# Optimization experiments

Hardware: AMD Instinct MI355X
Metric: run time of the kernel (lower is better)

Reference implementation:

```python
import jax, jax.numpy as jnp
import numpy as np
import math

B, S, D = 4, 4096, 2048
HEAD_DIM = 128  # dim_model // head_nums = 2048 // 16
DEPTH = 12


def setup_inputs() -> dict:
    key = jax.random.key(0)
    ks = jax.random.split(key, 8)
    std = 0.1
    return {
        "x": jax.random.normal(ks[0], (B, S, D), dtype=jnp.float32),
        "WQ": jax.random.normal(ks[1], (D, 2 * HEAD_DIM), dtype=jnp.float32) * (D ** -0.5),
        "WK": jax.random.normal(ks[2], (D, 2 * HEAD_DIM), dtype=jnp.float32) * (D ** -0.5),
        "WV": jax.random.normal(ks[3], (D, 2 * HEAD_DIM), dtype=jnp.float32) * (D ** -0.5),
        "lambda_q1": jax.random.normal(ks[4], (HEAD_DIM,), dtype=jnp.float32) * std,
        "lambda_q2": jax.random.normal(ks[5], (HEAD_DIM,), dtype=jnp.float32) * std,
        "lambda_k1": jax.random.normal(ks[6], (HEAD_DIM,), dtype=jnp.float32) * std,
        "lambda_k2": jax.random.normal(ks[7], (HEAD_DIM,), dtype=jnp.float32) * std,
    }


def reference(x, WQ, WK, WV, lambda_q1, lambda_q2, lambda_k1, lambda_k2):
    scale = HEAD_DIM ** -0.5
    lambda_init = 0.8 - 0.6 * math.exp(-0.3 * DEPTH)

    q = x @ WQ                      # [B, S, 2*hd]
    k = x @ WK
    v = x @ WV                      # [B, S, 2*hd]
    q1, q2 = q[..., :HEAD_DIM], q[..., HEAD_DIM:]
    k1, k2 = k[..., :HEAD_DIM], k[..., HEAD_DIM:]

    a1 = jnp.einsum("bqd,bkd->bqk", q1, k1) * scale  # [B, S, S]
    a2 = jnp.einsum("bqd,bkd->bqk", q2, k2) * scale

    lambda_1 = jnp.exp(jnp.sum(lambda_q1 * lambda_k1))
    lambda_2 = jnp.exp(jnp.sum(lambda_q2 * lambda_k2))
    lam = lambda_1 + lambda_2 + lambda_init

    attn = jax.nn.softmax(a1, axis=-1) - lam * jax.nn.softmax(a2, axis=-1)
    return jnp.einsum("bqk,bkd->bqd", attn, v)  # [B, S, 2*hd]
```

## Files before the change

kernel.cpp:

```cpp
#include <hip/hip_runtime.h>
#include <stdint.h>

typedef unsigned short u16;
typedef __attribute__((ext_vector_type(4))) float f32x4;
typedef __attribute__((ext_vector_type(16))) float f32x16;
typedef __attribute__((ext_vector_type(8))) short s16x8;
typedef __attribute__((ext_vector_type(8))) __bf16 bf16x8;
typedef __attribute__((ext_vector_type(8))) unsigned short u16x8;
typedef __attribute__((ext_vector_type(4))) unsigned short u16x4;

__device__ __forceinline__ f32x4 mfma16(s16x8 a, s16x8 b, f32x4 c) {
  return __builtin_amdgcn_mfma_f32_16x16x32_bf16(
      __builtin_bit_cast(bf16x8, a), __builtin_bit_cast(bf16x8, b), c, 0, 0, 0);
}
__device__ __forceinline__ f32x16 mfma32(s16x8 a, s16x8 b, f32x16 c) {
  return __builtin_amdgcn_mfma_f32_32x32x16_bf16(
      __builtin_bit_cast(bf16x8, a), __builtin_bit_cast(bf16x8, b), c, 0, 0, 0);
}

__device__ __forceinline__ void gl_lds16(const u16* g, u16* l) {
  __builtin_amdgcn_global_load_lds(
      (const __attribute__((address_space(1))) void*)g,
      (__attribute__((address_space(3))) void*)l, 16, 0, 0);
}

__device__ __forceinline__ u16 bf16rne(float f) {
  uint32_t u = __builtin_bit_cast(uint32_t, f);
  u += 0x7fffu + ((u >> 16) & 1u);
  return (u16)(u >> 16);
}

__global__ void cast_x_kernel(const float* __restrict__ x, u16* __restrict__ xb) {
  size_t i = ((size_t)blockIdx.x * 256 + threadIdx.x) * 8;
  f32x4 a = *(const f32x4*)(x + i);
  f32x4 b = *(const f32x4*)(x + i + 4);
  u16x8 o;
#pragma unroll
  for (int j = 0; j < 4; ++j) { o[j] = bf16rne(a[j]); o[4 + j] = bf16rne(b[j]); }
  *(u16x8*)(xb + i) = o;
}

__global__ void cast_w_kernel(const float* __restrict__ WQ, const float* __restrict__ WK,
                              const float* __restrict__ WV, u16* __restrict__ Wt, float qscale) {
  int i = blockIdx.x * 256 + threadIdx.x;
  int r = i >> 11, k = i & 2047;
  int sel = r >> 8, c = r & 255;
  const float* W = (sel == 0) ? WQ : (sel == 1) ? WK : WV;
  float v = W[(size_t)k * 256 + c];
  if (sel == 0) v *= qscale;
  Wt[i] = bf16rne(v);
}

__global__ __launch_bounds__(256) void proj_gemm(const u16* __restrict__ xb, const u16* __restrict__ Wt,
                                                 u16* __restrict__ Qb, u16* __restrict__ Kb,
                                                 u16* __restrict__ Vt) {
  const int bid = blockIdx.x;
  const int xcd = bid & 7, j = bid >> 3;
  const int m0 = (xcd * 16 + (j / 6)) * 128;
  const int n0 = (j % 6) * 128;
  const int tid = threadIdx.x, lane = tid & 63, w = tid >> 6;
  const int ln = lane & 15, quad = lane >> 4;
  const int wm = w & 1, wn = w >> 1;
  __shared__ __align__(16) u16 As[128 * 32];
  __shared__ __align__(16) u16 Bs[128 * 32];
  f32x4 acc[4][4];
#pragma unroll
  for (int i = 0; i < 4; ++i)
#pragma unroll
    for (int jj = 0; jj < 4; ++jj) acc[i][jj] = f32x4{0.f, 0.f, 0.f, 0.f};

  for (int kk = 0; kk < 2048; kk += 32) {
    __syncthreads();
#pragma unroll
    for (int i = 0; i < 2; ++i) {
      int p = tid + i * 256;
      int row = p >> 2, cg = (p & 3) ^ (row & 3);
      gl_lds16(xb + (size_t)(m0 + row) * 2048 + kk + cg * 8, As + (size_t)(p - lane) * 8);
      gl_lds16(Wt + (size_t)(n0 + row) * 2048 + kk + cg * 8, Bs + (size_t)(p - lane) * 8);
    }
    __syncthreads();
    s16x8 a[4];
#pragma unroll
    for (int mt = 0; mt < 4; ++mt) {
      int r = wm * 64 + mt * 16 + ln;
      a[mt] = *(const s16x8*)(As + r * 32 + ((quad ^ (r & 3)) * 8));
    }
#pragma unroll
    for (int nt = 0; nt < 4; ++nt) {
      int r = wn * 64 + nt * 16 + ln;
      s16x8 bf = *(const s16x8*)(Bs + r * 32 + ((quad ^ (r & 3)) * 8));
#pragma unroll
      for (int mt = 0; mt < 4; ++mt) acc[mt][nt] = mfma16(a[mt], bf, acc[mt][nt]);
    }
  }
#pragma unroll
  for (int mt = 0; mt < 4; ++mt)
#pragma unroll
    for (int nt = 0; nt < 4; ++nt) {
      int row0 = m0 + wm * 64 + mt * 16 + quad * 4;
      int col = n0 + wn * 64 + nt * 16 + ln;
      int sel = col >> 8, c = col & 255;
      u16x4 vv;
#pragma unroll
      for (int jj = 0; jj < 4; ++jj) vv[jj] = bf16rne(acc[mt][nt][jj]);
      if (sel == 2) {
        int b = row0 >> 12, s = row0 & 4095;
        *(u16x4*)(Vt + (size_t)b * 1048576 + (size_t)c * 4096 + s) = vv;
      } else {
        u16* dst = (sel == 0) ? Qb : Kb;
#pragma unroll
        for (int jj = 0; jj < 4; ++jj) dst[(size_t)(row0 + jj) * 256 + c] = vv[jj];
      }
    }
}

__global__ void lam_kernel(const float* __restrict__ lq1, const float* __restrict__ lq2,
                           const float* __restrict__ lk1, const float* __restrict__ lk2,
                           float* __restrict__ lamp) {
  int t = threadIdx.x;
  float d1 = lq1[t] * lk1[t] + lq1[t + 64] * lk1[t + 64];
  float d2 = lq2[t] * lk2[t] + lq2[t + 64] * lk2[t + 64];
#pragma unroll
  for (int off = 32; off; off >>= 1) {
    d1 += __shfl_xor(d1, off);
    d2 += __shfl_xor(d2, off);
  }
  if (t == 0) *lamp = expf(d1) + expf(d2) + (0.8f - 0.6f * expf(-3.6f));
}

__global__ __launch_bounds__(256, 2) void attn_kernel(const u16* __restrict__ Qb,
                                                      const u16* __restrict__ Kb,
                                                      const u16* __restrict__ Vt,
                                                      float* __restrict__ Op,
                                                      float* __restrict__ lp) {
  const int qt = blockIdx.x, half = blockIdx.y, b = blockIdx.z;
  const int tid = threadIdx.x, lane = tid & 63, w = tid >> 6;
  const int l5 = lane & 31, lh = lane >> 5;
  const int mapsel = w & 1, rt = w >> 1;

  __shared__ __align__(16) u16 Ks[64 * 256];
  __shared__ __align__(16) u16 Vs[256 * 64];
  u16* Ps = Ks;

  s16x8 aq[8];
  {
    const u16* qp = Qb + ((size_t)(b * 4096 + qt * 64 + rt * 32 + l5)) * 256 +
                    mapsel * 128 + lh * 8;
#pragma unroll
    for (int st = 0; st < 8; ++st) aq[st] = *(const s16x8*)(qp + st * 16);
  }

  f32x16 O[2][4];
#pragma unroll
  for (int i = 0; i < 2; ++i)
#pragma unroll
    for (int jj = 0; jj < 4; ++jj)
#pragma unroll
      for (int r = 0; r < 16; ++r) O[i][jj][r] = 0.f;
  float l_run[16];
#pragma unroll
  for (int r = 0; r < 16; ++r) l_run[r] = 0.f;

  const u16* Kg0 = Kb + ((size_t)b * 4096) * 256;
  const u16* Vg0 = Vt + (size_t)b * 1048576;
  const int kb0 = half * 2048;

  for (int kb = kb0; kb < kb0 + 2048; kb += 64) {
    __syncthreads();
#pragma unroll
    for (int i = 0; i < 8; ++i) {
      int p = tid + i * 256;
      int row = p >> 5, c = p & 31;
      int cg = (c & 16) | ((c ^ row) & 15);
      gl_lds16(Kg0 + (size_t)(kb + row) * 256 + cg * 8, Ks + (size_t)(p - lane) * 8);
    }
#pragma unroll
    for (int i = 0; i < 8; ++i) {
      int p = tid + i * 256;
      int row = p >> 3, c = p & 7;
      int cg = c ^ (row & 7);
      gl_lds16(Vg0 + (size_t)row * 4096 + kb + cg * 8, Vs + (size_t)(p - lane) * 8);
    }
    __syncthreads();

    f32x16 S0, S1;
#pragma unroll
    for (int r = 0; r < 16; ++r) { S0[r] = 0.f; S1[r] = 0.f; }
#pragma unroll
    for (int st = 0; st < 8; ++st) {
      int c = mapsel * 16 + st * 2 + lh;
      int ph0 = (c & 16) | ((c ^ l5) & 15);
      s16x8 b0 = *(const s16x8*)(Ks + l5 * 256 + ph0 * 8);
      s16x8 b1 = *(const s16x8*)(Ks + (32 + l5) * 256 + ph0 * 8);
      S0 = mfma32(aq[st], b0, S0);
      S1 = mfma32(aq[st], b1, S1);
    }

    __syncthreads();
    {
      int qbase = mapsel * 64 + rt * 32 + 4 * lh;
#pragma unroll
      for (int r = 0; r < 16; ++r) {
        float p0 = exp2f(S0[r]);
        float p1 = exp2f(S1[r]);
        l_run[r] += p0 + p1;
        int qrow = qbase + (r & 3) + 8 * (r >> 2);
        Ps[qrow * 72 + l5] = bf16rne(p0);
        Ps[qrow * 72 + 32 + l5] = bf16rne(p1);
      }
    }
    __syncthreads();

#pragma unroll
    for (int ks = 0; ks < 4; ++ks) {
      s16x8 ap0 = *(const s16x8*)(Ps + (mapsel * 64 + l5) * 72 + ks * 16 + lh * 8);
      s16x8 ap1 = *(const s16x8*)(Ps + (mapsel * 64 + 32 + l5) * 72 + ks * 16 + lh * 8);
      int c = ks * 2 + lh;
#pragma unroll
      for (int ct = 0; ct < 4; ++ct) {
        int n = (w >> 1) * 128 + ct * 32 + l5;
        s16x8 bv = *(const s16x8*)(Vs + n * 64 + ((c ^ (n & 7)) * 8));
        O[0][ct] = mfma32(ap0, bv, O[0][ct]);
        O[1][ct] = mfma32(ap1, bv, O[1][ct]);
      }
    }
  }

#pragma unroll
  for (int off = 16; off; off >>= 1)
#pragma unroll
    for (int r = 0; r < 16; ++r) l_run[r] += __shfl_xor(l_run[r], off);

  const int mh = mapsel * 2 + half;
  const size_t MS = (size_t)16384 * 256;
  float* Og = Op + (size_t)mh * MS + (size_t)b * 4096 * 256;
  float* lg = lp + (size_t)mh * 16384 + (size_t)b * 4096;
  if (l5 == 0) {
#pragma unroll
    for (int r = 0; r < 16; ++r) {
      int qg = qt * 64 + rt * 32 + 4 * lh + (r & 3) + 8 * (r >> 2);
      lg[qg] = l_run[r];
    }
  }
#pragma unroll
  for (int rt2 = 0; rt2 < 2; ++rt2)
#pragma unroll
    for (int ct = 0; ct < 4; ++ct)
#pragma unroll
      for (int r = 0; r < 16; ++r) {
        int qg = qt * 64 + rt2 * 32 + (r & 3) + 8 * (r >> 2) + 4 * lh;
        int col = (w >> 1) * 128 + ct * 32 + l5;
        Og[(size_t)qg * 256 + col] = O[rt2][ct][r];
      }
}

__global__ void combine_kernel(const float* __restrict__ Op, const float* __restrict__ lp,
                               const float* __restrict__ lamp, float* __restrict__ out) {
  size_t i = ((size_t)blockIdx.x * 256 + threadIdx.x) * 4;
  size_t row = i >> 8;
  const size_t MS = (size_t)16384 * 256;
  float lam = *lamp;
  float r1 = 1.f / (lp[row] + lp[16384 + row]);
  float r2 = 1.f / (lp[2 * 16384 + row] + lp[3 * 16384 + row]);
  f32x4 a0 = *(const f32x4*)(Op + i);
  f32x4 a1 = *(const f32x4*)(Op + MS + i);
  f32x4 b0 = *(const f32x4*)(Op + 2 * MS + i);
  f32x4 b1 = *(const f32x4*)(Op + 3 * MS + i);
  f32x4 r;
#pragma unroll
  for (int j = 0; j < 4; ++j) r[j] = (a0[j] + a1[j]) * r1 - lam * (b0[j] + b1[j]) * r2;
  *(f32x4*)(out + i) = r;
}

extern "C" void kernel_launch(void* const* d_in, const int* in_sizes, int n_in,
                              void* d_out, int out_size, void* d_ws, size_t ws_size,
                              hipStream_t stream) {
  (void)in_sizes; (void)n_in; (void)out_size; (void)ws_size;
  const float* x   = (const float*)d_in[0];
  const float* WQ  = (const float*)d_in[1];
  const float* WK  = (const float*)d_in[2];
  const float* WV  = (const float*)d_in[3];
  const float* lq1 = (const float*)d_in[4];
  const float* lq2 = (const float*)d_in[5];
  const float* lk1 = (const float*)d_in[6];
  const float* lk2 = (const float*)d_in[7];
  float* out = (float*)d_out;

  char* ws = (char*)d_ws;
  u16* xb = (u16*)ws;   ws += (size_t)16384 * 2048 * 2;
  u16* Wt = (u16*)ws;   ws += (size_t)768 * 2048 * 2;
  u16* Qb = (u16*)ws;   ws += (size_t)16384 * 256 * 2;
  u16* Kb = (u16*)ws;   ws += (size_t)16384 * 256 * 2;
  u16* Vt = (u16*)ws;   ws += (size_t)16384 * 256 * 2;
  float* Op = (float*)ws; ws += (size_t)4 * 16384 * 256 * 4;
  float* lp = (float*)ws; ws += (size_t)4 * 16384 * 4;
  float* lamp = (float*)ws;

  const float qscale = 0.0883883476f * 1.44269504f;

  hipLaunchKernelGGL(cast_x_kernel, dim3(16384), dim3(256), 0, stream, x, xb);
  hipLaunchKernelGGL(cast_w_kernel, dim3(6144), dim3(256), 0, stream, WQ, WK, WV, Wt, qscale);
  hipLaunchKernelGGL(proj_gemm, dim3(768), dim3(256), 0, stream, xb, Wt, Qb, Kb, Vt);
  hipLaunchKernelGGL(lam_kernel, dim3(1), dim3(64), 0, stream, lq1, lq2, lk1, lk2, lamp);
  hipLaunchKernelGGL(attn_kernel, dim3(64, 2, 4), dim3(256), 0, stream, Qb, Kb, Vt, Op, lp);
  hipLaunchKernelGGL(combine_kernel, dim3(4096), dim3(256), 0, stream, Op, lp, lamp, out);
}
```

Before: 475.0 us.

## Fuse split-K combine into attention and keep P in registers via transposed scores

The attention kernel now gives each block 32 queries over the full key range. It computes scores transposed (keys × queries), so the exponentiated probabilities can feed the PV MFMA straight from registers after a lane-swap shuffle, with no LDS round trip or extra barriers. The two softmax maps and two key halves are reduced in shared memory, normalised, combined with lambda and written straight to the output. This removes the fp32 partial-output buffers, their global traffic and the separate combine kernel. In exchange each block streams twice as many K/V tiles, and the block index is remapped so each batch is grouped per XCD.

```diff
diff --git a/kernel.cpp b/kernel.cpp
--- a/kernel.cpp
+++ b/kernel.cpp
@@ -8,6 +8,7 @@
 typedef __attribute__((ext_vector_type(8))) __bf16 bf16x8;
 typedef __attribute__((ext_vector_type(8))) unsigned short u16x8;
 typedef __attribute__((ext_vector_type(4))) unsigned short u16x4;
+typedef __attribute__((ext_vector_type(4))) uint32_t u32x4;
 
 __device__ __forceinline__ f32x4 mfma16(s16x8 a, s16x8 b, f32x4 c) {
   return __builtin_amdgcn_mfma_f32_16x16x32_bf16(
@@ -131,41 +132,41 @@
 __global__ __launch_bounds__(256, 2) void attn_kernel(const u16* __restrict__ Qb,
                                                       const u16* __restrict__ Kb,
                                                       const u16* __restrict__ Vt,
-                                                      float* __restrict__ Op,
-                                                      float* __restrict__ lp) {
-  const int qt = blockIdx.x, half = blockIdx.y, b = blockIdx.z;
+                                                      const float* __restrict__ lamp,
+                                                      float* __restrict__ out) {
+  const int bid = blockIdx.x;
+  const int xcd = bid & 7;
+  const int b = xcd >> 1;
+  const int qt = ((bid >> 3) << 1) + (xcd & 1);
   const int tid = threadIdx.x, lane = tid & 63, w = tid >> 6;
   const int l5 = lane & 31, lh = lane >> 5;
-  const int mapsel = w & 1, rt = w >> 1;
-
-  __shared__ __align__(16) u16 Ks[64 * 256];
-  __shared__ __align__(16) u16 Vs[256 * 64];
-  u16* Ps = Ks;
-
-  s16x8 aq[8];
+  const int m = w & 1, kt = w >> 1;
+
+  __shared__ __align__(16) char smem[68096];
+  u16* Ks = (u16*)smem;
+  u16* Vs = (u16*)(smem + 32768);
+  float* buf0 = (float*)smem;
+  float* buf1 = (float*)(smem + 33792);
+  float* ls = (float*)(smem + 67584);
+
+  s16x8 bq[8];
   {
-    const u16* qp = Qb + ((size_t)(b * 4096 + qt * 64 + rt * 32 + l5)) * 256 +
-                    mapsel * 128 + lh * 8;
-#pragma unroll
-    for (int st = 0; st < 8; ++st) aq[st] = *(const s16x8*)(qp + st * 16);
-  }
-
-  f32x16 O[2][4];
-#pragma unroll
-  for (int i = 0; i < 2; ++i)
-#pragma unroll
-    for (int jj = 0; jj < 4; ++jj)
-#pragma unroll
-      for (int r = 0; r < 16; ++r) O[i][jj][r] = 0.f;
-  float l_run[16];
-#pragma unroll
-  for (int r = 0; r < 16; ++r) l_run[r] = 0.f;
+    const u16* qp = Qb + ((size_t)(b * 4096 + qt * 32 + l5)) * 256 + m * 128 + lh * 8;
+#pragma unroll
+    for (int s = 0; s < 8; ++s) bq[s] = *(const s16x8*)(qp + s * 16);
+  }
+
+  f32x16 O[8];
+#pragma unroll
+  for (int ct = 0; ct < 8; ++ct)
+#pragma unroll
+    for (int r = 0; r < 16; ++r) O[ct][r] = 0.f;
+  float l_run = 0.f;
 
   const u16* Kg0 = Kb + ((size_t)b * 4096) * 256;
   const u16* Vg0 = Vt + (size_t)b * 1048576;
-  const int kb0 = half * 2048;
-
-  for (int kb = kb0; kb < kb0 + 2048; kb += 64) {
+
+  for (int kb = 0; kb < 4096; kb += 64) {
     __syncthreads();
 #pragma unroll
     for (int i = 0; i < 8; ++i) {
@@ -183,93 +184,82 @@
     }
     __syncthreads();
 
-    f32x16 S0, S1;
-#pragma unroll
-    for (int r = 0; r < 16; ++r) { S0[r] = 0.f; S1[r] = 0.f; }
-#pragma unroll
-    for (int st = 0; st < 8; ++st) {
-      int c = mapsel * 16 + st * 2 + lh;
-      int ph0 = (c & 16) | ((c ^ l5) & 15);
-      s16x8 b0 = *(const s16x8*)(Ks + l5 * 256 + ph0 * 8);
-      s16x8 b1 = *(const s16x8*)(Ks + (32 + l5) * 256 + ph0 * 8);
-      S0 = mfma32(aq[st], b0, S0);
-      S1 = mfma32(aq[st], b1, S1);
-    }
-
-    __syncthreads();
-    {
-      int qbase = mapsel * 64 + rt * 32 + 4 * lh;
+    f32x16 Sa, Sb;
+#pragma unroll
+    for (int r = 0; r < 16; ++r) { Sa[r] = 0.f; Sb[r] = 0.f; }
+#pragma unroll
+    for (int s = 0; s < 8; s += 2) {
+      int row = kt * 32 + l5;
+      int c0 = m * 16 + s * 2 + lh;
+      int c1 = m * 16 + (s + 1) * 2 + lh;
+      s16x8 a0 = *(const s16x8*)(Ks + row * 256 + (((c0 & 16) | ((c0 ^ row) & 15))) * 8);
+      s16x8 a1 = *(const s16x8*)(Ks + row * 256 + (((c1 & 16) | ((c1 ^ row) & 15))) * 8);
+      Sa = mfma32(a0, bq[s], Sa);
+      Sb = mfma32(a1, bq[s + 1], Sb);
+    }
+
+    uint32_t P[8];
+#pragma unroll
+    for (int d = 0; d < 8; ++d) {
+      float p0 = exp2f(Sa[2 * d] + Sb[2 * d]);
+      float p1 = exp2f(Sa[2 * d + 1] + Sb[2 * d + 1]);
+      l_run += p0 + p1;
+      P[d] = (uint32_t)bf16rne(p0) | ((uint32_t)bf16rne(p1) << 16);
+    }
+    uint32_t X[8];
+#pragma unroll
+    for (int d = 0; d < 8; ++d) X[d] = (uint32_t)__shfl_xor((int)P[d], 32);
+
+#pragma unroll
+    for (int ks = 0; ks < 2; ++ks) {
+      u32x4 fd;
+      fd[0] = lh ? X[ks * 4 + 2] : P[ks * 4 + 0];
+      fd[1] = lh ? X[ks * 4 + 3] : P[ks * 4 + 1];
+      fd[2] = lh ? P[ks * 4 + 2] : X[ks * 4 + 0];
+      fd[3] = lh ? P[ks * 4 + 3] : X[ks * 4 + 1];
+      s16x8 pf = __builtin_bit_cast(s16x8, fd);
+      int c = (kt * 32 + ks * 16) / 8 + lh;
+#pragma unroll
+      for (int ct = 0; ct < 8; ++ct) {
+        int row = ct * 32 + l5;
+        s16x8 vf = *(const s16x8*)(Vs + row * 64 + ((c ^ (row & 7)) * 8));
+        O[ct] = mfma32(vf, pf, O[ct]);
+      }
+    }
+  }
+
+  float lam = *lamp;
+  l_run += __shfl_xor(l_run, 32);
+  __syncthreads();
+  if (lane < 32) ls[(m * 2 + kt) * 32 + l5] = l_run;
+  float* bufm = m ? buf1 : buf0;
+  if (kt == 1) {
+#pragma unroll
+    for (int ct = 0; ct < 8; ++ct)
 #pragma unroll
       for (int r = 0; r < 16; ++r) {
-        float p0 = exp2f(S0[r]);
-        float p1 = exp2f(S1[r]);
-        l_run[r] += p0 + p1;
-        int qrow = qbase + (r & 3) + 8 * (r >> 2);
-        Ps[qrow * 72 + l5] = bf16rne(p0);
-        Ps[qrow * 72 + 32 + l5] = bf16rne(p1);
-      }
-    }
-    __syncthreads();
-
-#pragma unroll
-    for (int ks = 0; ks < 4; ++ks) {
-      s16x8 ap0 = *(const s16x8*)(Ps + (mapsel * 64 + l5) * 72 + ks * 16 + lh * 8);
-      s16x8 ap1 = *(const s16x8*)(Ps + (mapsel * 64 + 32 + l5) * 72 + ks * 16 + lh * 8);
-      int c = ks * 2 + lh;
-#pragma unroll
-      for (int ct = 0; ct < 4; ++ct) {
-        int n = (w >> 1) * 128 + ct * 32 + l5;
-        s16x8 bv = *(const s16x8*)(Vs + n * 64 + ((c ^ (n & 7)) * 8));
-        O[0][ct] = mfma32(ap0, bv, O[0][ct]);
-        O[1][ct] = mfma32(ap1, bv, O[1][ct]);
-      }
-    }
-  }
-
-#pragma unroll
-  for (int off = 16; off; off >>= 1)
-#pragma unroll
-    for (int r = 0; r < 16; ++r) l_run[r] += __shfl_xor(l_run[r], off);
-
-  const int mh = mapsel * 2 + half;
-  const size_t MS = (size_t)16384 * 256;
-  float* Og = Op + (size_t)mh * MS + (size_t)b * 4096 * 256;
-  float* lg = lp + (size_t)mh * 16384 + (size_t)b * 4096;
-  if (l5 == 0) {
-#pragma unroll
-    for (int r = 0; r < 16; ++r) {
-      int qg = qt * 64 + rt * 32 + 4 * lh + (r & 3) + 8 * (r >> 2);
-      lg[qg] = l_run[r];
-    }
-  }
-#pragma unroll
-  for (int rt2 = 0; rt2 < 2; ++rt2)
-#pragma unroll
-    for (int ct = 0; ct < 4; ++ct)
+        int vcol = ct * 32 + (r & 3) + 8 * (r >> 2) + 4 * lh;
+        bufm[vcol * 33 + l5] = O[ct][r];
+      }
+  }
+  __syncthreads();
+  if (kt == 0) {
+    float linv = 1.f / (ls[(m * 2) * 32 + l5] + ls[(m * 2 + 1) * 32 + l5]);
+#pragma unroll
+    for (int ct = 0; ct < 8; ++ct)
 #pragma unroll
       for (int r = 0; r < 16; ++r) {
-        int qg = qt * 64 + rt2 * 32 + (r & 3) + 8 * (r >> 2) + 4 * lh;
-        int col = (w >> 1) * 128 + ct * 32 + l5;
-        Og[(size_t)qg * 256 + col] = O[rt2][ct][r];
-      }
-}
-
-__global__ void combine_kernel(const float* __restrict__ Op, const float* __restrict__ lp,
-                               const float* __restrict__ lamp, float* __restrict__ out) {
-  size_t i = ((size_t)blockIdx.x * 256 + threadIdx.x) * 4;
-  size_t row = i >> 8;
-  const size_t MS = (size_t)16384 * 256;
-  float lam = *lamp;
-  float r1 = 1.f / (lp[row] + lp[16384 + row]);
-  float r2 = 1.f / (lp[2 * 16384 + row] + lp[3 * 16384 + row]);
-  f32x4 a0 = *(const f32x4*)(Op + i);
-  f32x4 a1 = *(const f32x4*)(Op + MS + i);
-  f32x4 b0 = *(const f32x4*)(Op + 2 * MS + i);
-  f32x4 b1 = *(const f32x4*)(Op + 3 * MS + i);
-  f32x4 r;
-#pragma unroll
-  for (int j = 0; j < 4; ++j) r[j] = (a0[j] + a1[j]) * r1 - lam * (b0[j] + b1[j]) * r2;
-  *(f32x4*)(out + i) = r;
+        int vcol = ct * 32 + (r & 3) + 8 * (r >> 2) + 4 * lh;
+        bufm[vcol * 33 + l5] = (O[ct][r] + bufm[vcol * 33 + l5]) * linv;
+      }
+  }
+  __syncthreads();
+  float* og = out + ((size_t)(b * 4096 + qt * 32)) * 256;
+#pragma unroll
+  for (int j2 = 0; j2 < 32; ++j2) {
+    float v = buf0[tid * 33 + j2] - lam * buf1[tid * 33 + j2];
+    og[(size_t)j2 * 256 + tid] = v;
+  }
 }
 
 extern "C" void kernel_launch(void* const* d_in, const int* in_sizes, int n_in,
@@ -292,8 +282,6 @@
   u16* Qb = (u16*)ws;   ws += (size_t)16384 * 256 * 2;
   u16* Kb = (u16*)ws;   ws += (size_t)16384 * 256 * 2;
   u16* Vt = (u16*)ws;   ws += (size_t)16384 * 256 * 2;
-  float* Op = (float*)ws; ws += (size_t)4 * 16384 * 256 * 4;
-  float* lp = (float*)ws; ws += (size_t)4 * 16384 * 4;
   float* lamp = (float*)ws;
 
   const float qscale = 0.0883883476f * 1.44269504f;
@@ -302,6 +290,5 @@
   hipLaunchKernelGGL(cast_w_kernel, dim3(6144), dim3(256), 0, stream, WQ, WK, WV, Wt, qscale);
   hipLaunchKernelGGL(proj_gemm, dim3(768), dim3(256), 0, stream, xb, Wt, Qb, Kb, Vt);
   hipLaunchKernelGGL(lam_kernel, dim3(1), dim3(64), 0, stream, lq1, lq2, lk1, lk2, lamp);
-  hipLaunchKernelGGL(attn_kernel, dim3(64, 2, 4), dim3(256), 0, stream, Qb, Kb, Vt, Op, lp);
-  hipLaunchKernelGGL(combine_kernel, dim3(4096), dim3(256), 0, stream, Op, lp, lamp, out);
-}
+  hipLaunchKernelGGL(attn_kernel, dim3(512), dim3(256), 0, stream, Qb, Kb, Vt, lamp, out);
+}
```

Result: faster. 430.3 us (-9.4%).
